# Kernel tuning notes

Measured on AMD Instinct MI355X. Metric: run time of the kernel, lower is better.

## Reference

```python
import jax, jax.numpy as jnp
import numpy as np

E, D, H = 8, 512, 2048  # num_experts, features, features*mlp_ratio
B, S = 4, 512


def _lecun(key, shape):
    fan_in = shape[-2] if len(shape) >= 2 else shape[0]
    return jax.random.normal(key, shape, dtype=jnp.float32) / jnp.sqrt(jnp.float32(fan_in))


def setup_inputs() -> dict:
    key = jax.random.key(0)
    ks = jax.random.split(key, 8)
    return {
        'x_real': jax.random.normal(ks[0], (B, S, D), dtype=jnp.float32),
        'x_imag': jax.random.normal(ks[1], (B, S, D), dtype=jnp.float32),
        # gating Dense over concat([amp, phase]) -> in_features = 2*D
        'gate_W': _lecun(ks[2], (2 * D, E)),
        'gate_b': jnp.zeros((E,), jnp.float32),
        # per-expert ComplexLinear 1: D -> H
        'W1r': _lecun(ks[3], (E, D, H)),
        'W1i': _lecun(ks[4], (E, D, H)),
        'b1r': jnp.zeros((E, H), jnp.float32),
        'b1i': jnp.zeros((E, H), jnp.float32),
        # per-expert ComplexModReLU bias
        'mod_b': jnp.zeros((E, H), jnp.float32),
        # per-expert ComplexLinear 2: H -> D
        'W2r': _lecun(ks[5], (E, H, D)),
        'W2i': _lecun(ks[6], (E, H, D)),
        'b2r': jnp.zeros((E, D), jnp.float32),
        'b2i': jnp.zeros((E, D), jnp.float32),
    }


def reference(x_real, x_imag, gate_W, gate_b, W1r, W1i, b1r, b1i, mod_b, W2r, W2i, b2r, b2i):
    eps = 1e-10
    # --- gating: scores over [|z|, angle(z)] ---
    amp = jnp.sqrt(x_real ** 2 + x_imag ** 2)            # |z|, [B,S,D]
    phase = jnp.arctan2(x_imag, x_real)                  # angle(z)
    routing_input = jnp.concatenate([amp, phase], axis=-1)  # [B,S,2D]
    scores = routing_input @ gate_W + gate_b             # [B,S,E]
    probs = jax.nn.softmax(scores, axis=-1)
    idx = jnp.argmax(probs, axis=-1)                     # [B,S] top-1 expert

    # --- all experts dense (faithful to reference): complex linear 1 ---
    # (Wr + iWi)(xr + ixi) : hr = xr Wr - xi Wi ; hi = xr Wi + xi Wr
    h_r = (jnp.einsum('bsd,edh->ebsh', x_real, W1r)
           - jnp.einsum('bsd,edh->ebsh', x_imag, W1i)) + b1r[:, None, None, :]
    h_i = (jnp.einsum('bsd,edh->ebsh', x_real, W1i)
           + jnp.einsum('bsd,edh->ebsh', x_imag, W1r)) + b1i[:, None, None, :]

    # --- ComplexModReLU: relu(|z|+b) * z / (|z|+eps), |z| = sqrt(r^2+i^2+eps) ---
    a = jnp.sqrt(h_r ** 2 + h_i ** 2 + eps)              # [E,B,S,H]
    scale = jax.nn.relu(a + mod_b[:, None, None, :]) / (a + eps)
    h_r = h_r * scale
    h_i = h_i * scale

    # --- complex linear 2 ---
    o_r = (jnp.einsum('ebsh,ehd->ebsd', h_r, W2r)
           - jnp.einsum('ebsh,ehd->ebsd', h_i, W2i)) + b2r[:, None, None, :]
    o_i = (jnp.einsum('ebsh,ehd->ebsd', h_r, W2i)
           + jnp.einsum('ebsh,ehd->ebsd', h_i, W2r)) + b2i[:, None, None, :]

    # --- mask + weight (top-1): out = sum_e out_e * probs[...,e] * (argmax==e) ---
    e_ids = jnp.arange(probs.shape[-1])
    w = jnp.transpose(probs, (2, 0, 1)) * (idx[None, :, :] == e_ids[:, None, None])  # [E,B,S]
    out_r = jnp.einsum('ebs,ebsd->bsd', w, o_r)
    out_i = jnp.einsum('ebs,ebsd->bsd', w, o_i)
    return (out_r, out_i)
```

## Files before the change

### kernel.cpp

```cpp
#include <hip/hip_runtime.h>
#include <math.h>

#define NE 8
#define ND 512
#define NH 2048
#define NT 2048
#define MAXIT 40

typedef __attribute__((ext_vector_type(8))) short short8;
typedef __attribute__((ext_vector_type(4))) float f32x4;

#define GLL(g, d) __builtin_amdgcn_global_load_lds( \
    (const __attribute__((address_space(1))) void*)(g), \
    (__attribute__((address_space(3))) void*)(d), 16, 0, 0)

__device__ __forceinline__ unsigned short f2bf(float x) {
    unsigned int u = __builtin_bit_cast(unsigned int, x);
    u += 0x7FFFu + ((u >> 16) & 1u);
    return (unsigned short)(u >> 16);
}

__device__ __forceinline__ short8 lds8(const unsigned short* p) {
    return *(const short8*)p;
}

__global__ __launch_bounds__(256) void gate_kernel(
    const float* __restrict__ xr, const float* __restrict__ xi,
    const float* __restrict__ gW, const float* __restrict__ gb,
    float* __restrict__ gate_w,
    int* __restrict__ counts, int* __restrict__ tok_list,
    unsigned short* __restrict__ obr, unsigned short* __restrict__ obi)
{
    int t = blockIdx.x;
    int tid = threadIdx.x;
    const float* xrt = xr + (size_t)t * ND;
    const float* xit = xi + (size_t)t * ND;

    #pragma unroll
    for (int d = tid; d < ND; d += 256) {
        obr[(size_t)t * ND + d] = f2bf(xrt[d]);
        obi[(size_t)t * ND + d] = f2bf(xit[d]);
    }

    float acc[NE] = {0,0,0,0,0,0,0,0};
    for (int r = tid; r < 2 * ND; r += 256) {
        int d = r & (ND - 1);
        float a = xrt[d], b = xit[d];
        float v = (r < ND) ? sqrtf(a * a + b * b) : atan2f(b, a);
        const float4* g = (const float4*)(gW + (size_t)r * NE);
        float4 g0 = g[0], g1 = g[1];
        acc[0] += v * g0.x; acc[1] += v * g0.y; acc[2] += v * g0.z; acc[3] += v * g0.w;
        acc[4] += v * g1.x; acc[5] += v * g1.y; acc[6] += v * g1.z; acc[7] += v * g1.w;
    }
    #pragma unroll
    for (int e = 0; e < NE; e++) {
        for (int off = 32; off > 0; off >>= 1)
            acc[e] += __shfl_down(acc[e], off, 64);
    }
    __shared__ float part[4][NE];
    int wave = tid >> 6, lane = tid & 63;
    if (lane == 0) {
        #pragma unroll
        for (int e = 0; e < NE; e++) part[wave][e] = acc[e];
    }
    __syncthreads();
    if (tid == 0) {
        float s[NE];
        #pragma unroll
        for (int e = 0; e < NE; e++)
            s[e] = part[0][e] + part[1][e] + part[2][e] + part[3][e] + gb[e];
        int amax = 0; float m = s[0];
        #pragma unroll
        for (int e = 1; e < NE; e++) if (s[e] > m) { m = s[e]; amax = e; }
        float denom = 0.f;
        #pragma unroll
        for (int e = 0; e < NE; e++) denom += expf(s[e] - m);
        gate_w[t] = 1.0f / denom;
        int pos = atomicAdd(&counts[amax], 1);
        tok_list[amax * NT + pos] = t;
    }
}

__global__ __launch_bounds__(256) void transw_kernel(
    const float* __restrict__ W1r, unsigned short* __restrict__ w1tr,
    const float* __restrict__ W1i, unsigned short* __restrict__ w1ti,
    const float* __restrict__ W2r, unsigned short* __restrict__ w2tr,
    const float* __restrict__ W2i, unsigned short* __restrict__ w2ti,
    int* __restrict__ counts)
{
    __shared__ unsigned short tile[64][72];
    int z = blockIdx.z;
    int e = z & 7, which = z >> 3;
    if (z == 0 && blockIdx.x == 0 && blockIdx.y == 0 && threadIdx.x < 16)
        counts[threadIdx.x] = 0;
    int R = which ? NH : ND;
    int C = which ? ND : NH;
    int c0 = (which ? blockIdx.y : blockIdx.x) * 64;
    int r0 = (which ? blockIdx.x : blockIdx.y) * 64;
    const float* s0 = which ? W2r : W1r;
    const float* s1 = which ? W2i : W1i;
    unsigned short* d0 = which ? w2tr : w1tr;
    unsigned short* d1 = which ? w2ti : w1ti;
    size_t off = (size_t)e * R * C;
    int tid = threadIdx.x;
    #pragma unroll
    for (int p = 0; p < 2; ++p) {
        const float* src = (p ? s1 : s0) + off;
        unsigned short* dst = (p ? d1 : d0) + off;
        if (p) __syncthreads();
        #pragma unroll
        for (int i = 0; i < 4; ++i) {
            int r = i * 16 + (tid >> 4);
            int c4 = (tid & 15) * 4;
            float4 v = *(const float4*)&src[(size_t)(r0 + r) * C + c0 + c4];
            tile[c4 + 0][r] = f2bf(v.x);
            tile[c4 + 1][r] = f2bf(v.y);
            tile[c4 + 2][r] = f2bf(v.z);
            tile[c4 + 3][r] = f2bf(v.w);
        }
        __syncthreads();
        #pragma unroll
        for (int i = 0; i < 2; ++i) {
            int c = i * 32 + (tid >> 3);
            int r8 = (tid & 7) * 8;
            short8 v = *(const short8*)&tile[c][r8];
            *(short8*)&dst[(size_t)(c0 + c) * R + r0 + r8] = v;
        }
    }
}


#define VMW16 asm volatile("s_waitcnt vmcnt(16)" ::: "memory")
#define VMW8  asm volatile("s_waitcnt vmcnt(8)"  ::: "memory")
#define VMW0  asm volatile("s_waitcnt vmcnt(0)"  ::: "memory")
#define BARX do {                            \
    __builtin_amdgcn_sched_barrier(0);       \
    __builtin_amdgcn_s_barrier();            \
    __builtin_amdgcn_sched_barrier(0);       \
} while (0)
#define SP1 __builtin_amdgcn_s_setprio(1)
#define SP0 __builtin_amdgcn_s_setprio(0)

#define RING_DECL __shared__ alignas(16) unsigned short ring[4][16384];

#define STAGE_S(s, ko) do {                                  \
    unsigned short* _b = &ring[s][0];                        \
    GLL(gAr0 + (ko), _b + (w * 16) * 64);                    \
    GLL(gAr1 + (ko), _b + (w * 16 + 8) * 64);                \
    GLL(gAi0 + (ko), _b + 4096 + (w * 16) * 64);             \
    GLL(gAi1 + (ko), _b + 4096 + (w * 16 + 8) * 64);         \
    GLL(gBr0 + (ko), _b + 8192 + (w * 16) * 64);             \
    GLL(gBr1 + (ko), _b + 8192 + (w * 16 + 8) * 64);         \
    GLL(gBi0 + (ko), _b + 12288 + (w * 16) * 64);            \
    GLL(gBi1 + (ko), _b + 12288 + (w * 16 + 8) * 64);        \
} while (0)

#define COMPUTE_S(s) do {                                                        \
    const unsigned short* _sa = &ring[s][0];                                     \
    _Pragma("unroll")                                                            \
    for (int ks = 0; ks < 2; ++ks) {                                             \
        int pa = ((ks * 4 + quad) ^ (l15 & 7)) * 8;                              \
        short8 br  = lds8(_sa + 8192  + (w * 16 + l15) * 64 + pa);               \
        short8 bi2 = lds8(_sa + 12288 + (w * 16 + l15) * 64 + pa);               \
        _Pragma("unroll")                                                        \
        for (int m = 0; m < 4; ++m) {                                            \
            short8 ar  = lds8(_sa + (m * 16 + l15) * 64 + pa);                   \
            short8 ai2 = lds8(_sa + 4096 + (m * 16 + l15) * 64 + pa);            \
            aRR[m] = __builtin_amdgcn_mfma_f32_16x16x32_bf16(ar,  br,  aRR[m], 0, 0, 0); \
            aII[m] = __builtin_amdgcn_mfma_f32_16x16x32_bf16(ai2, bi2, aII[m], 0, 0, 0); \
            aRI[m] = __builtin_amdgcn_mfma_f32_16x16x32_bf16(ar,  bi2, aRI[m], 0, 0, 0); \
            aIR[m] = __builtin_amdgcn_mfma_f32_16x16x32_bf16(ai2, br,  aIR[m], 0, 0, 0); \
        }                                                                        \
    }                                                                            \
} while (0)

#define PIPE_RING(NK) do {                                                   \
    STAGE_S(0, 0); STAGE_S(1, 64); STAGE_S(2, 128);                          \
    _Pragma("unroll 1")                                                      \
    for (int t = 0; t < (NK) - 3; ++t) {                                     \
        VMW16; BARX;                                                         \
        STAGE_S((t + 3) & 3, (t + 3) * 64);                                  \
        SP1; COMPUTE_S(t & 3); SP0;                                          \
    }                                                                        \
    VMW16; BARX; SP1; COMPUTE_S(((NK) - 3) & 3); SP0;                        \
    VMW8;  BARX; SP1; COMPUTE_S(((NK) - 2) & 3); SP0;                        \
    VMW0;  BARX; SP1; COMPUTE_S(((NK) - 1) & 3); SP0;                        \
} while (0)

__device__ __forceinline__ bool find_item(const int* counts, int item,
                                          int& e, int& mt, int& n) {
    int rem = item;
    for (e = 0; e < NE; ++e) {
        n = counts[e];
        int m = (n + 63) >> 6;
        if (rem < m) { mt = rem; return true; }
        rem -= m;
    }
    return false;
}

__global__ __launch_bounds__(256, 1) void moe1_kernel(
    const unsigned short* __restrict__ xbr, const unsigned short* __restrict__ xbi,
    const unsigned short* __restrict__ w1tr, const unsigned short* __restrict__ w1ti,
    const float* __restrict__ b1r, const float* __restrict__ b1i,
    const float* __restrict__ mod_b,
    const int* __restrict__ counts, const int* __restrict__ tok_list,
    unsigned short* __restrict__ hr, unsigned short* __restrict__ hi)
{
    int bid = blockIdx.x;
    int xg = bid & 7, tg = bid >> 3;
    int nt = tg & 31;
    int item = (tg >> 5) * 8 + xg;
    int e, mt, n;
    if (!find_item(counts, item, e, mt, n)) return;
    int mbase = mt * 64, n0 = nt * 64;

    int tid = threadIdx.x;
    int w = tid >> 6, l = tid & 63;
    int l15 = l & 15, quad = l >> 4;
    int swz = (((l & 7) ^ ((l >> 3) & 7)) * 8);

    RING_DECL

    const int* tl = tok_list + e * NT;
    int ia0 = mbase + w * 16 + (l >> 3);
    int ia1 = ia0 + 8;
    int ra0 = tl[ia0 < n ? ia0 : n - 1];
    int ra1 = tl[ia1 < n ? ia1 : n - 1];
    const unsigned short* gAr0 = xbr + (size_t)ra0 * ND + swz;
    const unsigned short* gAi0 = xbi + (size_t)ra0 * ND + swz;
    const unsigned short* gAr1 = xbr + (size_t)ra1 * ND + swz;
    const unsigned short* gAi1 = xbi + (size_t)ra1 * ND + swz;
    size_t brow = (size_t)e * NH + n0 + w * 16 + (l >> 3);
    const unsigned short* gBr0 = w1tr + brow * ND + swz;
    const unsigned short* gBr1 = w1tr + (brow + 8) * ND + swz;
    const unsigned short* gBi0 = w1ti + brow * ND + swz;
    const unsigned short* gBi1 = w1ti + (brow + 8) * ND + swz;

    f32x4 aRR[4] = {}, aII[4] = {}, aRI[4] = {}, aIR[4] = {};

    PIPE_RING(ND / 64);

    int col = n0 + w * 16 + l15;
    float bre = b1r[(size_t)e * NH + col];
    float bie = b1i[(size_t)e * NH + col];
    float mbv = mod_b[(size_t)e * NH + col];
    #pragma unroll
    for (int m = 0; m < 4; ++m) {
        #pragma unroll
        for (int r = 0; r < 4; ++r) {
            int tix = m * 16 + quad * 4 + r;
            if (mbase + tix >= n) continue;
            int tok = tl[mbase + tix];
            float vr = aRR[m][r] - aII[m][r] + bre;
            float vi = aRI[m][r] + aIR[m][r] + bie;
            float a = sqrtf(vr * vr + vi * vi + 1e-10f);
            float sc = fmaxf(a + mbv, 0.0f) / (a + 1e-10f);
            hr[(size_t)tok * NH + col] = f2bf(vr * sc);
            hi[(size_t)tok * NH + col] = f2bf(vi * sc);
        }
    }
}

__global__ __launch_bounds__(256, 1) void moe2_kernel(
    const unsigned short* __restrict__ hr, const unsigned short* __restrict__ hi,
    const unsigned short* __restrict__ w2tr, const unsigned short* __restrict__ w2ti,
    const float* __restrict__ b2r, const float* __restrict__ b2i,
    const int* __restrict__ counts, const int* __restrict__ tok_list,
    const float* __restrict__ gate_w,
    float* __restrict__ out)
{
    int bid = blockIdx.x;
    int xg = bid & 7, tg = bid >> 3;
    int nt = tg & 7;
    int item = (tg >> 3) * 8 + xg;
    int e, mt, n;
    if (!find_item(counts, item, e, mt, n)) return;
    int mbase = mt * 64, n0 = nt * 64;

    int tid = threadIdx.x;
    int w = tid >> 6, l = tid & 63;
    int l15 = l & 15, quad = l >> 4;
    int swz = (((l & 7) ^ ((l >> 3) & 7)) * 8);

    RING_DECL

    const int* tl = tok_list + e * NT;
    int ia0 = mbase + w * 16 + (l >> 3);
    int ia1 = ia0 + 8;
    int ra0 = tl[ia0 < n ? ia0 : n - 1];
    int ra1 = tl[ia1 < n ? ia1 : n - 1];
    const unsigned short* gAr0 = hr + (size_t)ra0 * NH + swz;
    const unsigned short* gAi0 = hi + (size_t)ra0 * NH + swz;
    const unsigned short* gAr1 = hr + (size_t)ra1 * NH + swz;
    const unsigned short* gAi1 = hi + (size_t)ra1 * NH + swz;
    size_t brow = (size_t)e * ND + n0 + w * 16 + (l >> 3);
    const unsigned short* gBr0 = w2tr + brow * NH + swz;
    const unsigned short* gBr1 = w2tr + (brow + 8) * NH + swz;
    const unsigned short* gBi0 = w2ti + brow * NH + swz;
    const unsigned short* gBi1 = w2ti + (brow + 8) * NH + swz;

    f32x4 aRR[4] = {}, aII[4] = {}, aRI[4] = {}, aIR[4] = {};

    PIPE_RING(NH / 64);

    int col = n0 + w * 16 + l15;
    float bre = b2r[(size_t)e * ND + col];
    float bie = b2i[(size_t)e * ND + col];
    #pragma unroll
    for (int m = 0; m < 4; ++m) {
        #pragma unroll
        for (int r = 0; r < 4; ++r) {
            int tix = m * 16 + quad * 4 + r;
            if (mbase + tix >= n) continue;
            int tok = tl[mbase + tix];
            float gw = gate_w[tok];
            out[(size_t)tok * ND + col] = (aRR[m][r] - aII[m][r] + bre) * gw;
            out[(size_t)NT * ND + (size_t)tok * ND + col] = (aRI[m][r] + aIR[m][r] + bie) * gw;
        }
    }
}

extern "C" void kernel_launch(void* const* d_in, const int* in_sizes, int n_in,
                              void* d_out, int out_size, void* d_ws, size_t ws_size,
                              hipStream_t stream) {
    const float* xr   = (const float*)d_in[0];
    const float* xi   = (const float*)d_in[1];
    const float* gW   = (const float*)d_in[2];
    const float* gb   = (const float*)d_in[3];
    const float* W1r  = (const float*)d_in[4];
    const float* W1i  = (const float*)d_in[5];
    const float* b1r  = (const float*)d_in[6];
    const float* b1i  = (const float*)d_in[7];
    const float* modb = (const float*)d_in[8];
    const float* W2r  = (const float*)d_in[9];
    const float* W2i  = (const float*)d_in[10];
    const float* b2r  = (const float*)d_in[11];
    const float* b2i  = (const float*)d_in[12];
    float* out = (float*)d_out;

    char* ws = (char*)d_ws;
    int*   counts   = (int*)ws;
    float* gate_w   = (float*)(ws + 256);
    int*   tok_list = (int*)(ws + 256 + 8192);
    size_t off = 256 + 8192 + (size_t)NE * NT * 4;
    unsigned short* xbr  = (unsigned short*)(ws + off); off += (size_t)NT * ND * 2;
    unsigned short* xbi  = (unsigned short*)(ws + off); off += (size_t)NT * ND * 2;
    unsigned short* w1tr = (unsigned short*)(ws + off); off += (size_t)NE * ND * NH * 2;
    unsigned short* w1ti = (unsigned short*)(ws + off); off += (size_t)NE * ND * NH * 2;
    unsigned short* w2tr = (unsigned short*)(ws + off); off += (size_t)NE * ND * NH * 2;
    unsigned short* w2ti = (unsigned short*)(ws + off); off += (size_t)NE * ND * NH * 2;
    unsigned short* h_r  = (unsigned short*)(ws + off); off += (size_t)NT * NH * 2;
    unsigned short* h_i  = (unsigned short*)(ws + off); off += (size_t)NT * NH * 2;

    transw_kernel<<<dim3(32, 8, 16), 256, 0, stream>>>(
        W1r, w1tr, W1i, w1ti, W2r, w2tr, W2i, w2ti, counts);
    gate_kernel<<<NT, 256, 0, stream>>>(xr, xi, gW, gb, gate_w, counts, tok_list, xbr, xbi);
    moe1_kernel<<<8 * 32 * (MAXIT / 8), 256, 0, stream>>>(
        xbr, xbi, w1tr, w1ti, b1r, b1i, modb, counts, tok_list, h_r, h_i);
    moe2_kernel<<<8 * 8 * (MAXIT / 8), 256, 0, stream>>>(
        h_r, h_i, w2tr, w2ti, b2r, b2i, counts, tok_list, gate_w, out);
}
```

Baseline: 336.4 us.

## Replace 4-stage 64-K ring with 2-stage 32-K double buffer for higher occupancy

Replaces the 4-deep LDS ring of 64-wide K tiles (128 KB) with a 2-buffer double buffer of 32-wide K tiles (32 KB). This lets launch_bounds request 5 blocks per CU instead of 1, so latency is hidden by other resident blocks rather than a deep per-block prefetch. The load-to-LDS swizzle and the read permutation are redone to match the new 32-wide layout. In exchange there are twice as many K iterations, each with two barriers, and only one tile in flight per block.

```diff
diff --git a/kernel.cpp b/kernel.cpp
--- a/kernel.cpp
+++ b/kernel.cpp
@@ -130,8 +130,7 @@
 }
 
 
-#define VMW16 asm volatile("s_waitcnt vmcnt(16)" ::: "memory")
-#define VMW8  asm volatile("s_waitcnt vmcnt(8)"  ::: "memory")
+#define VMW4  asm volatile("s_waitcnt vmcnt(4)"  ::: "memory")
 #define VMW0  asm volatile("s_waitcnt vmcnt(0)"  ::: "memory")
 #define BARX do {                            \
     __builtin_amdgcn_sched_barrier(0);       \
@@ -141,50 +140,38 @@
 #define SP1 __builtin_amdgcn_s_setprio(1)
 #define SP0 __builtin_amdgcn_s_setprio(0)
 
-#define RING_DECL __shared__ alignas(16) unsigned short ring[4][16384];
-
-#define STAGE_S(s, ko) do {                                  \
-    unsigned short* _b = &ring[s][0];                        \
-    GLL(gAr0 + (ko), _b + (w * 16) * 64);                    \
-    GLL(gAr1 + (ko), _b + (w * 16 + 8) * 64);                \
-    GLL(gAi0 + (ko), _b + 4096 + (w * 16) * 64);             \
-    GLL(gAi1 + (ko), _b + 4096 + (w * 16 + 8) * 64);         \
-    GLL(gBr0 + (ko), _b + 8192 + (w * 16) * 64);             \
-    GLL(gBr1 + (ko), _b + 8192 + (w * 16 + 8) * 64);         \
-    GLL(gBi0 + (ko), _b + 12288 + (w * 16) * 64);            \
-    GLL(gBi1 + (ko), _b + 12288 + (w * 16 + 8) * 64);        \
+#define MOE_LDS_DECL __shared__ alignas(16) unsigned short LBUF[2][4][2048];
+
+#define STAGE_(b, ko) do {                      \
+    GLL(gAr + (ko), &LBUF[b][0][w * 512]);      \
+    GLL(gAi + (ko), &LBUF[b][1][w * 512]);      \
+    GLL(gBr + (ko), &LBUF[b][2][w * 512]);      \
+    GLL(gBi + (ko), &LBUF[b][3][w * 512]);      \
 } while (0)
 
-#define COMPUTE_S(s) do {                                                        \
-    const unsigned short* _sa = &ring[s][0];                                     \
+#define COMPUTE_(s) do {                                                         \
+    short8 br  = lds8(&LBUF[s][2][w * 512 + P8]);                                \
+    short8 bi2 = lds8(&LBUF[s][3][w * 512 + P8]);                                \
     _Pragma("unroll")                                                            \
-    for (int ks = 0; ks < 2; ++ks) {                                             \
-        int pa = ((ks * 4 + quad) ^ (l15 & 7)) * 8;                              \
-        short8 br  = lds8(_sa + 8192  + (w * 16 + l15) * 64 + pa);               \
-        short8 bi2 = lds8(_sa + 12288 + (w * 16 + l15) * 64 + pa);               \
-        _Pragma("unroll")                                                        \
-        for (int m = 0; m < 4; ++m) {                                            \
-            short8 ar  = lds8(_sa + (m * 16 + l15) * 64 + pa);                   \
-            short8 ai2 = lds8(_sa + 4096 + (m * 16 + l15) * 64 + pa);            \
-            aRR[m] = __builtin_amdgcn_mfma_f32_16x16x32_bf16(ar,  br,  aRR[m], 0, 0, 0); \
-            aII[m] = __builtin_amdgcn_mfma_f32_16x16x32_bf16(ai2, bi2, aII[m], 0, 0, 0); \
-            aRI[m] = __builtin_amdgcn_mfma_f32_16x16x32_bf16(ar,  bi2, aRI[m], 0, 0, 0); \
-            aIR[m] = __builtin_amdgcn_mfma_f32_16x16x32_bf16(ai2, br,  aIR[m], 0, 0, 0); \
-        }                                                                        \
+    for (int m = 0; m < 4; ++m) {                                                \
+        short8 ar  = lds8(&LBUF[s][0][m * 512 + P8]);                            \
+        short8 ai2 = lds8(&LBUF[s][1][m * 512 + P8]);                            \
+        aRR[m] = __builtin_amdgcn_mfma_f32_16x16x32_bf16(ar,  br,  aRR[m], 0, 0, 0); \
+        aII[m] = __builtin_amdgcn_mfma_f32_16x16x32_bf16(ai2, bi2, aII[m], 0, 0, 0); \
+        aRI[m] = __builtin_amdgcn_mfma_f32_16x16x32_bf16(ar,  bi2, aRI[m], 0, 0, 0); \
+        aIR[m] = __builtin_amdgcn_mfma_f32_16x16x32_bf16(ai2, br,  aIR[m], 0, 0, 0); \
     }                                                                            \
 } while (0)
 
-#define PIPE_RING(NK) do {                                                   \
-    STAGE_S(0, 0); STAGE_S(1, 64); STAGE_S(2, 128);                          \
+#define PIPE2(NK) do {                                                       \
+    STAGE_(0, 0); VMW0; BARX;                                                \
     _Pragma("unroll 1")                                                      \
-    for (int t = 0; t < (NK) - 3; ++t) {                                     \
-        VMW16; BARX;                                                         \
-        STAGE_S((t + 3) & 3, (t + 3) * 64);                                  \
-        SP1; COMPUTE_S(t & 3); SP0;                                          \
+    for (int kt = 0; kt < (NK); kt += 2) {                                   \
+        if (kt + 1 < (NK)) { STAGE_(1, (kt + 1) * 32); VMW4; } else VMW0;    \
+        BARX; SP1; COMPUTE_(0); SP0; BARX;                                   \
+        if (kt + 2 < (NK)) { STAGE_(0, (kt + 2) * 32); VMW4; } else VMW0;    \
+        BARX; SP1; COMPUTE_(1); SP0; BARX;                                   \
     }                                                                        \
-    VMW16; BARX; SP1; COMPUTE_S(((NK) - 3) & 3); SP0;                        \
-    VMW8;  BARX; SP1; COMPUTE_S(((NK) - 2) & 3); SP0;                        \
-    VMW0;  BARX; SP1; COMPUTE_S(((NK) - 1) & 3); SP0;                        \
 } while (0)
 
 __device__ __forceinline__ bool find_item(const int* counts, int item,
@@ -199,7 +186,16 @@
     return false;
 }
 
-__global__ __launch_bounds__(256, 1) void moe1_kernel(
+#define MOE_IDX_DECL                                                   \
+    int tid = threadIdx.x;                                             \
+    int w = tid >> 6, l = tid & 63;                                    \
+    int l15 = l & 15, quad = l >> 4;                                   \
+    int rl = (l >> 2) ^ ((l >> 4) & 1);                                \
+    int ql = (l & 3) ^ (rl & 3);                                       \
+    int qoff = ql * 8;                                                 \
+    int P8 = (((l15 * 4 + (quad ^ (l15 & 3))) ^ (l15 & 4)) * 8);
+
+__global__ __launch_bounds__(256, 5) void moe1_kernel(
     const unsigned short* __restrict__ xbr, const unsigned short* __restrict__ xbi,
     const unsigned short* __restrict__ w1tr, const unsigned short* __restrict__ w1ti,
     const float* __restrict__ b1r, const float* __restrict__ b1i,
@@ -215,31 +211,21 @@
     if (!find_item(counts, item, e, mt, n)) return;
     int mbase = mt * 64, n0 = nt * 64;
 
-    int tid = threadIdx.x;
-    int w = tid >> 6, l = tid & 63;
-    int l15 = l & 15, quad = l >> 4;
-    int swz = (((l & 7) ^ ((l >> 3) & 7)) * 8);
-
-    RING_DECL
+    MOE_IDX_DECL
+    MOE_LDS_DECL
 
     const int* tl = tok_list + e * NT;
-    int ia0 = mbase + w * 16 + (l >> 3);
-    int ia1 = ia0 + 8;
-    int ra0 = tl[ia0 < n ? ia0 : n - 1];
-    int ra1 = tl[ia1 < n ? ia1 : n - 1];
-    const unsigned short* gAr0 = xbr + (size_t)ra0 * ND + swz;
-    const unsigned short* gAi0 = xbi + (size_t)ra0 * ND + swz;
-    const unsigned short* gAr1 = xbr + (size_t)ra1 * ND + swz;
-    const unsigned short* gAi1 = xbi + (size_t)ra1 * ND + swz;
-    size_t brow = (size_t)e * NH + n0 + w * 16 + (l >> 3);
-    const unsigned short* gBr0 = w1tr + brow * ND + swz;
-    const unsigned short* gBr1 = w1tr + (brow + 8) * ND + swz;
-    const unsigned short* gBi0 = w1ti + brow * ND + swz;
-    const unsigned short* gBi1 = w1ti + (brow + 8) * ND + swz;
+    int ia = mbase + w * 16 + rl;
+    int ra = tl[ia < n ? ia : n - 1];
+    const unsigned short* gAr = xbr + (size_t)ra * ND + qoff;
+    const unsigned short* gAi = xbi + (size_t)ra * ND + qoff;
+    size_t brow = (size_t)e * NH + n0 + w * 16 + rl;
+    const unsigned short* gBr = w1tr + brow * ND + qoff;
+    const unsigned short* gBi = w1ti + brow * ND + qoff;
 
     f32x4 aRR[4] = {}, aII[4] = {}, aRI[4] = {}, aIR[4] = {};
 
-    PIPE_RING(ND / 64);
+    PIPE2(ND / 32);
 
     int col = n0 + w * 16 + l15;
     float bre = b1r[(size_t)e * NH + col];
@@ -262,7 +248,7 @@
     }
 }
 
-__global__ __launch_bounds__(256, 1) void moe2_kernel(
+__global__ __launch_bounds__(256, 5) void moe2_kernel(
     const unsigned short* __restrict__ hr, const unsigned short* __restrict__ hi,
     const unsigned short* __restrict__ w2tr, const unsigned short* __restrict__ w2ti,
     const float* __restrict__ b2r, const float* __restrict__ b2i,
@@ -278,31 +264,21 @@
     if (!find_item(counts, item, e, mt, n)) return;
     int mbase = mt * 64, n0 = nt * 64;
 
-    int tid = threadIdx.x;
-    int w = tid >> 6, l = tid & 63;
-    int l15 = l & 15, quad = l >> 4;
-    int swz = (((l & 7) ^ ((l >> 3) & 7)) * 8);
-
-    RING_DECL
+    MOE_IDX_DECL
+    MOE_LDS_DECL
 
     const int* tl = tok_list + e * NT;
-    int ia0 = mbase + w * 16 + (l >> 3);
-    int ia1 = ia0 + 8;
-    int ra0 = tl[ia0 < n ? ia0 : n - 1];
-    int ra1 = tl[ia1 < n ? ia1 : n - 1];
-    const unsigned short* gAr0 = hr + (size_t)ra0 * NH + swz;
-    const unsigned short* gAi0 = hi + (size_t)ra0 * NH + swz;
-    const unsigned short* gAr1 = hr + (size_t)ra1 * NH + swz;
-    const unsigned short* gAi1 = hi + (size_t)ra1 * NH + swz;
-    size_t brow = (size_t)e * ND + n0 + w * 16 + (l >> 3);
-    const unsigned short* gBr0 = w2tr + brow * NH + swz;
-    const unsigned short* gBr1 = w2tr + (brow + 8) * NH + swz;
-    const unsigned short* gBi0 = w2ti + brow * NH + swz;
-    const unsigned short* gBi1 = w2ti + (brow + 8) * NH + swz;
+    int ia = mbase + w * 16 + rl;
+    int ra = tl[ia < n ? ia : n - 1];
+    const unsigned short* gAr = hr + (size_t)ra * NH + qoff;
+    const unsigned short* gAi = hi + (size_t)ra * NH + qoff;
+    size_t brow = (size_t)e * ND + n0 + w * 16 + rl;
+    const unsigned short* gBr = w2tr + brow * NH + qoff;
+    const unsigned short* gBi = w2ti + brow * NH + qoff;
 
     f32x4 aRR[4] = {}, aII[4] = {}, aRI[4] = {}, aIR[4] = {};
 
-    PIPE_RING(NH / 64);
+    PIPE2(NH / 32);
 
     int col = n0 + w * 16 + l15;
     float bre = b2r[(size_t)e * ND + col];
```

After: 368.4 us. +9.5%, slower.
